# Kernel tuning notes

Hardware: AMD Instinct MI355X
Metric: run time of the kernel (lower is better)

The kernel has to match this reference:

```python
import jax, jax.numpy as jnp
import numpy as np

B, S, H = 4, 2048, 1024
NH = 16
HD = H // NH  # 64


def setup_inputs() -> dict:
    key = jax.random.key(0)
    ks = jax.random.split(key, 9)
    s = 1.0 / np.sqrt(H)
    inp = {
        "x": jax.random.normal(ks[0], (B, S, H), dtype=jnp.float32),
        "wq": jax.random.normal(ks[1], (H, H), dtype=jnp.float32) * s,
        "bq": jnp.zeros((H,), dtype=jnp.float32),
        "wk": jax.random.normal(ks[2], (H, H), dtype=jnp.float32) * s,
        "bk": jnp.zeros((H,), dtype=jnp.float32),
        "wv": jax.random.normal(ks[3], (H, H), dtype=jnp.float32) * s,
        "bv": jnp.zeros((H,), dtype=jnp.float32),
        "wo": jax.random.normal(ks[4], (H, H), dtype=jnp.float32) * s,
        "bo": jnp.zeros((H,), dtype=jnp.float32),
    }
    return inp


def _split_heads(t):
    # [B,S,H] -> [B,NH,S,HD]
    return t.reshape(B, S, NH, HD).transpose(0, 2, 1, 3)


def reference(x, wq, bq, wk, bk, wv, bv, wo, bo):
    # Linear layers (torch Linear: x @ W^T + b; weights here stored as [in,out])
    q = _split_heads(x @ wq + bq)
    k = _split_heads(x @ wk + bk)
    v = _split_heads(x @ wv + bv)
    scale = 1.0 / jnp.sqrt(jnp.asarray(HD, dtype=x.dtype))
    scores = jnp.einsum("bhqd,bhkd->bhqk", q, k) * scale  # [B,NH,S,S]
    attn = jax.nn.softmax(scores, axis=-1)
    ctx = jnp.einsum("bhqk,bhkd->bhqd", attn, v)  # [B,NH,S,HD]
    ctx = ctx.transpose(0, 2, 1, 3).reshape(B, S, H)
    return ctx @ wo + bo
```

## Files before the change

kernel.cpp:

```cpp
#include <hip/hip_runtime.h>
#include <hip/hip_bf16.h>
#include <math.h>

typedef __bf16 bf16;
typedef __attribute__((ext_vector_type(4))) __bf16 bf16x4;
typedef __attribute__((ext_vector_type(8))) __bf16 bf16x8;
typedef __attribute__((ext_vector_type(4))) float f32x4;

#define B_  4
#define S_  2048
#define H_  1024
#define NH_ 16
#define HD_ 64
#define M_  (B_ * S_)

#define LP  72
#define LPV 136
#define KV_ 128

__device__ __forceinline__ f32x4 mfma16(bf16x8 a, bf16x8 b, f32x4 c) {
    return __builtin_amdgcn_mfma_f32_16x16x32_bf16(a, b, c, 0, 0, 0);
}

__device__ __forceinline__ void glds16(const bf16* g, bf16* l) {
    __builtin_amdgcn_global_load_lds(
        (const __attribute__((address_space(1))) void*)g,
        (__attribute__((address_space(3))) void*)l, 16, 0, 0);
}

__global__ __launch_bounds__(256) void cvt_bf16(const float* __restrict__ in,
                                                bf16* __restrict__ out) {
    const size_t i = ((size_t)blockIdx.x * 256 + threadIdx.x) * 8;
    float4 f0 = *(const float4*)&in[i];
    float4 f1 = *(const float4*)&in[i + 4];
    bf16x8 v;
    v[0] = (bf16)f0.x; v[1] = (bf16)f0.y; v[2] = (bf16)f0.z; v[3] = (bf16)f0.w;
    v[4] = (bf16)f1.x; v[5] = (bf16)f1.y; v[6] = (bf16)f1.z; v[7] = (bf16)f1.w;
    *(bf16x8*)&out[i] = v;
}

__global__ __launch_bounds__(256) void transpose_w4(const float* __restrict__ s0,
                                                    const float* __restrict__ s1,
                                                    const float* __restrict__ s2,
                                                    const float* __restrict__ s3,
                                                    bf16* __restrict__ d0,
                                                    bf16* __restrict__ d1,
                                                    bf16* __restrict__ d2,
                                                    bf16* __restrict__ d3) {
    __shared__ bf16 tile[64][65];
    const int z = blockIdx.z;
    const float* in = (z == 0) ? s0 : (z == 1) ? s1 : (z == 2) ? s2 : s3;
    bf16* out = (z == 0) ? d0 : (z == 1) ? d1 : (z == 2) ? d2 : d3;
    const int t = threadIdx.x;
    const int bx = blockIdx.x * 64, by = blockIdx.y * 64;
#pragma unroll
    for (int i = 0; i < 16; ++i) {
        int idx = i * 256 + t;
        int r = idx >> 6, c = idx & 63;
        tile[r][c] = (bf16)in[(by + r) * 1024 + bx + c];
    }
    __syncthreads();
#pragma unroll
    for (int i = 0; i < 16; ++i) {
        int idx = i * 256 + t;
        int r = idx >> 6, c = idx & 63;
        out[(bx + r) * 1024 + by + c] = tile[c][r];
    }
}

__global__ __launch_bounds__(256) void gemm_qkv(const bf16* __restrict__ A,
                                                const bf16* __restrict__ Bt,
                                                const float* __restrict__ b0,
                                                const float* __restrict__ b1,
                                                const float* __restrict__ b2,
                                                bf16* __restrict__ out0,
                                                bf16* __restrict__ out1,
                                                bf16* __restrict__ out2t,
                                                float scale0) {
    __shared__ alignas(16) bf16 As[128 * 64];
    __shared__ alignas(16) bf16 Bs[128 * 64];
    const int t = threadIdx.x;
    const int m0 = blockIdx.x * 128;
    const int n0 = blockIdx.y * 128;
    const int lane = t & 63, w = t >> 6;
    const int quad = lane >> 4, l15 = lane & 15;
    const int wm = w >> 1, wn = w & 1;
    const int srow = lane >> 3;
    const int scol = (lane & 7) * 8;

    const bf16* Ab = A + (size_t)(m0 + srow) * 1024 + scol;
    const bf16* Bb = Bt + (size_t)(n0 + srow) * 1024 + scol;

    f32x4 acc[4][4];
#pragma unroll
    for (int i = 0; i < 4; ++i)
#pragma unroll
        for (int j = 0; j < 4; ++j) acc[i][j] = (f32x4){0.f, 0.f, 0.f, 0.f};

    for (int kt = 0; kt < 16; ++kt) {
#pragma unroll
        for (int i = 0; i < 4; ++i) {
            const int c = w * 4 + i;
            glds16(Ab + (size_t)c * 8 * 1024 + kt * 64, &As[c * 512]);
            glds16(Bb + (size_t)c * 8 * 1024 + kt * 64, &Bs[c * 512]);
        }
        __syncthreads();
#pragma unroll
        for (int ks = 0; ks < 2; ++ks) {
            bf16x8 a[4], b[4];
#pragma unroll
            for (int mi = 0; mi < 4; ++mi)
                a[mi] = *(const bf16x8*)&As[(wm * 64 + mi * 16 + l15) * 64 + ks * 32 + quad * 8];
#pragma unroll
            for (int ni = 0; ni < 4; ++ni)
                b[ni] = *(const bf16x8*)&Bs[(wn * 64 + ni * 16 + l15) * 64 + ks * 32 + quad * 8];
#pragma unroll
            for (int mi = 0; mi < 4; ++mi)
#pragma unroll
                for (int ni = 0; ni < 4; ++ni)
                    acc[mi][ni] = mfma16(a[mi], b[ni], acc[mi][ni]);
        }
        __syncthreads();
    }

    const int seg = n0 >> 10;
    const float* bias = (seg == 0) ? b0 : (seg == 1) ? b1 : b2;
#pragma unroll
    for (int ni = 0; ni < 4; ++ni) {
        const int coln = (n0 & 1023) + wn * 64 + ni * 16 + l15;
        const float bcol = bias[coln];
#pragma unroll
        for (int mi = 0; mi < 4; ++mi) {
            const int row0 = m0 + wm * 64 + mi * 16 + quad * 4;
            if (seg == 2) {
                bf16x4 v;
#pragma unroll
                for (int r = 0; r < 4; ++r) v[r] = (bf16)(acc[mi][ni][r] + bcol);
                *(bf16x4*)&out2t[(size_t)coln * M_ + row0] = v;
            } else if (seg == 1) {
#pragma unroll
                for (int r = 0; r < 4; ++r)
                    out1[(size_t)(row0 + r) * 1024 + coln] = (bf16)(acc[mi][ni][r] + bcol);
            } else {
#pragma unroll
                for (int r = 0; r < 4; ++r)
                    out0[(size_t)(row0 + r) * 1024 + coln] =
                        (bf16)((acc[mi][ni][r] + bcol) * scale0);
            }
        }
    }
}

__global__ __launch_bounds__(256) void gemm_o(const bf16* __restrict__ A,
                                              const bf16* __restrict__ Bt,
                                              const float* __restrict__ b0,
                                              float* __restrict__ out0) {
    __shared__ alignas(16) bf16 As[128 * 64];
    __shared__ alignas(16) bf16 Bs[128 * 64];
    const int t = threadIdx.x;
    const int m0 = blockIdx.x * 128;
    const int n0 = blockIdx.y * 128;
    const int lane = t & 63, w = t >> 6;
    const int quad = lane >> 4, l15 = lane & 15;
    const int wm = w >> 1, wn = w & 1;
    const int srow = lane >> 3;
    const int scol = (lane & 7) * 8;

    const bf16* Ab = A + (size_t)(m0 + srow) * 1024 + scol;
    const bf16* Bb = Bt + (size_t)(n0 + srow) * 1024 + scol;

    f32x4 acc[4][4];
#pragma unroll
    for (int i = 0; i < 4; ++i)
#pragma unroll
        for (int j = 0; j < 4; ++j) acc[i][j] = (f32x4){0.f, 0.f, 0.f, 0.f};

    for (int kt = 0; kt < 16; ++kt) {
#pragma unroll
        for (int i = 0; i < 4; ++i) {
            const int c = w * 4 + i;
            glds16(Ab + (size_t)c * 8 * 1024 + kt * 64, &As[c * 512]);
            glds16(Bb + (size_t)c * 8 * 1024 + kt * 64, &Bs[c * 512]);
        }
        __syncthreads();
#pragma unroll
        for (int ks = 0; ks < 2; ++ks) {
            bf16x8 a[4], b[4];
#pragma unroll
            for (int mi = 0; mi < 4; ++mi)
                a[mi] = *(const bf16x8*)&As[(wm * 64 + mi * 16 + l15) * 64 + ks * 32 + quad * 8];
#pragma unroll
            for (int ni = 0; ni < 4; ++ni)
                b[ni] = *(const bf16x8*)&Bs[(wn * 64 + ni * 16 + l15) * 64 + ks * 32 + quad * 8];
#pragma unroll
            for (int mi = 0; mi < 4; ++mi)
#pragma unroll
                for (int ni = 0; ni < 4; ++ni)
                    acc[mi][ni] = mfma16(a[mi], b[ni], acc[mi][ni]);
        }
        __syncthreads();
    }

#pragma unroll
    for (int ni = 0; ni < 4; ++ni) {
        const int coln = n0 + wn * 64 + ni * 16 + l15;
        const float bcol = b0[coln];
#pragma unroll
        for (int mi = 0; mi < 4; ++mi) {
            const int row0 = m0 + wm * 64 + mi * 16 + quad * 4;
#pragma unroll
            for (int r = 0; r < 4; ++r)
                out0[(size_t)(row0 + r) * 1024 + coln] = acc[mi][ni][r] + bcol;
        }
    }
}

__global__ __launch_bounds__(256, 4) void attn(const bf16* Q,
                                               const bf16* __restrict__ K,
                                               const bf16* __restrict__ Vt,
                                               bf16* O) {
    __shared__ alignas(16) bf16 smem[128 * LP + 64 * LPV];
    bf16* Ks = smem;
    bf16* Vs = smem + 128 * LP;

    const int t = threadIdx.x;
    const int lane = t & 63, w = t >> 6;
    const int quad = lane >> 4, l15 = lane & 15;
    const int bh = blockIdx.x;
    const int q0 = blockIdx.y * 128;
    const int b = bh >> 4, h = bh & 15;
    const bf16* qp  = Q + (size_t)b * S_ * H_ + h * HD_;
    const bf16* kp  = K + (size_t)b * S_ * H_ + h * HD_;
    const bf16* vtp = Vt + (size_t)(h * HD_) * M_ + b * S_;

    const int rk = t >> 3;
    const int kc = (t & 7) * 8;
    const int skb = ((rk >> 2) & 1) * 16 + ((rk >> 3) & 3) * 4 + (rk & 3);
    const int vd0 = rk, vd1 = rk + 32;

    bf16x8 kpre[4], vpre[4];
#pragma unroll
    for (int j = 0; j < 4; ++j)
        kpre[j] = *(const bf16x8*)&kp[(size_t)(rk + 32 * j) * H_ + kc];
    vpre[0] = *(const bf16x8*)&vtp[(size_t)vd0 * M_ + kc];
    vpre[1] = *(const bf16x8*)&vtp[(size_t)vd0 * M_ + 64 + kc];
    vpre[2] = *(const bf16x8*)&vtp[(size_t)vd1 * M_ + kc];
    vpre[3] = *(const bf16x8*)&vtp[(size_t)vd1 * M_ + 64 + kc];

#pragma unroll
    for (int i = 0; i < 4; ++i) {
        int c = i * 256 + t;
        int row = c >> 3, qkc = (c & 7) * 8;
        *(bf16x8*)&smem[row * LP + qkc] =
            *(const bf16x8*)&qp[(size_t)(q0 + row) * H_ + qkc];
    }
    __syncthreads();
    bf16x8 aq[2][2];
#pragma unroll
    for (int mi = 0; mi < 2; ++mi)
#pragma unroll
        for (int ks = 0; ks < 2; ++ks)
            aq[mi][ks] = *(const bf16x8*)
                &smem[(w * 32 + mi * 16 + l15) * LP + ks * 32 + quad * 8];

    bf16x8 ones;
#pragma unroll
    for (int j = 0; j < 8; ++j) ones[j] = (bf16)1.0f;

    f32x4 o[2][4];
    f32x4 lsum[2];
#pragma unroll
    for (int mi = 0; mi < 2; ++mi) {
        lsum[mi] = (f32x4){0.f, 0.f, 0.f, 0.f};
#pragma unroll
        for (int i = 0; i < 4; ++i) o[mi][i] = (f32x4){0.f, 0.f, 0.f, 0.f};
    }

    for (int kt = 0; kt < S_ / KV_; ++kt) {
        __syncthreads();
#pragma unroll
        for (int j = 0; j < 4; ++j)
            *(bf16x8*)&Ks[(skb + 32 * j) * LP + kc] = kpre[j];
        *(bf16x8*)&Vs[vd0 * LPV + kc]      = vpre[0];
        *(bf16x8*)&Vs[vd0 * LPV + 64 + kc] = vpre[1];
        *(bf16x8*)&Vs[vd1 * LPV + kc]      = vpre[2];
        *(bf16x8*)&Vs[vd1 * LPV + 64 + kc] = vpre[3];
        __syncthreads();

        if (kt + 1 < S_ / KV_) {
            const int key1 = (kt + 1) * KV_;
#pragma unroll
            for (int j = 0; j < 4; ++j)
                kpre[j] = *(const bf16x8*)&kp[(size_t)(key1 + rk + 32 * j) * H_ + kc];
            vpre[0] = *(const bf16x8*)&vtp[(size_t)vd0 * M_ + key1 + kc];
            vpre[1] = *(const bf16x8*)&vtp[(size_t)vd0 * M_ + key1 + 64 + kc];
            vpre[2] = *(const bf16x8*)&vtp[(size_t)vd1 * M_ + key1 + kc];
            vpre[3] = *(const bf16x8*)&vtp[(size_t)vd1 * M_ + key1 + 64 + kc];
        }

#pragma unroll
        for (int ks = 0; ks < 4; ++ks) {
            bf16x8 k00 = *(const bf16x8*)&Ks[((2 * ks) * 16 + l15) * LP + quad * 8];
            bf16x8 k01 = *(const bf16x8*)&Ks[((2 * ks) * 16 + l15) * LP + 32 + quad * 8];
            bf16x8 k10 = *(const bf16x8*)&Ks[((2 * ks + 1) * 16 + l15) * LP + quad * 8];
            bf16x8 k11 = *(const bf16x8*)&Ks[((2 * ks + 1) * 16 + l15) * LP + 32 + quad * 8];
            f32x4 sA[2], sB[2];
#pragma unroll
            for (int mi = 0; mi < 2; ++mi) {
                sA[mi] = mfma16(k00, aq[mi][0], (f32x4){0.f, 0.f, 0.f, 0.f});
                sA[mi] = mfma16(k01, aq[mi][1], sA[mi]);
                sB[mi] = mfma16(k10, aq[mi][0], (f32x4){0.f, 0.f, 0.f, 0.f});
                sB[mi] = mfma16(k11, aq[mi][1], sB[mi]);
            }
            bf16x8 ap[2];
#pragma unroll
            for (int mi = 0; mi < 2; ++mi) {
                bf16x8 v;
#pragma unroll
                for (int j = 0; j < 4; ++j) v[j] = (bf16)__expf(sA[mi][j]);
#pragma unroll
                for (int j = 0; j < 4; ++j) v[4 + j] = (bf16)__expf(sB[mi][j]);
                ap[mi] = v;
            }
#pragma unroll
            for (int mi = 0; mi < 2; ++mi)
                lsum[mi] = mfma16(ap[mi], ones, lsum[mi]);
#pragma unroll
            for (int dt = 0; dt < 4; ++dt) {
                bf16x8 bv = *(const bf16x8*)&Vs[(dt * 16 + l15) * LPV + ks * 32 + quad * 8];
#pragma unroll
                for (int mi = 0; mi < 2; ++mi)
                    o[mi][dt] = mfma16(ap[mi], bv, o[mi][dt]);
            }
        }
    }

#pragma unroll
    for (int mi = 0; mi < 2; ++mi)
#pragma unroll
        for (int r = 0; r < 4; ++r) {
            float inv = 1.f / lsum[mi][r];
            int row = q0 + w * 32 + mi * 16 + quad * 4 + r;
            size_t base = (size_t)b * S_ * H_ + (size_t)row * H_ + h * HD_;
#pragma unroll
            for (int dt = 0; dt < 4; ++dt)
                O[base + dt * 16 + l15] = (bf16)(o[mi][dt][r] * inv);
        }
}

extern "C" void kernel_launch(void* const* d_in, const int* in_sizes, int n_in,
                              void* d_out, int out_size, void* d_ws, size_t ws_size,
                              hipStream_t stream) {
    const float* x  = (const float*)d_in[0];
    const float* wq = (const float*)d_in[1];
    const float* bq = (const float*)d_in[2];
    const float* wk = (const float*)d_in[3];
    const float* bk = (const float*)d_in[4];
    const float* wv = (const float*)d_in[5];
    const float* bv = (const float*)d_in[6];
    const float* wo = (const float*)d_in[7];
    const float* bo = (const float*)d_in[8];

    bf16* ws = (bf16*)d_ws;
    const size_t WSZ = 1024 * 1024;
    const size_t TSZ = (size_t)M_ * H_;
    bf16* wt  = ws;
    bf16* qb  = wt + WSZ;
    bf16* kb  = qb + TSZ;
    bf16* vbt = kb + TSZ;
    bf16* ctx = qb;

    bf16* xb    = (bf16*)d_out;
    bf16* wqkvt = xb + TSZ;

    cvt_bf16<<<dim3(M_ * H_ / (256 * 8)), 256, 0, stream>>>(x, xb);

    transpose_w4<<<dim3(16, 16, 4), 256, 0, stream>>>(
        wq, wk, wv, wo, wqkvt, wqkvt + WSZ, wqkvt + 2 * WSZ, wt);

    dim3 qkvgrid(M_ / 128, 3072 / 128);
    gemm_qkv<<<qkvgrid, 256, 0, stream>>>(xb, wqkvt, bq, bk, bv,
                                          qb, kb, vbt, 0.125f);

    dim3 agrid(B_ * NH_, S_ / 128);
    attn<<<agrid, 256, 0, stream>>>(qb, kb, vbt, ctx);

    dim3 ogrid(M_ / 128, 1024 / 128);
    gemm_o<<<ogrid, 256, 0, stream>>>(ctx, wt, bo, (float*)d_out);
}
```

Baseline: 280.9 us.

## Double-buffer 64-key attention tiles, use exp2 with folded log2e, add setprio

The attention kernel drops from 128-key single-buffered tiles with two barriers per iteration to 64-key tiles in a double-buffered LDS ring with one barrier per iteration. The Q scale now folds in log2(e) so softmax can use exp2 instead of expf. s_setprio raises wave priority around the MFMA phases. This aims to cut barrier stalls and exponent cost, but doubles the number of loop iterations.

Result: slower. 309.5 us (+10.2%).

```diff
diff --git a/kernel.cpp b/kernel.cpp
--- a/kernel.cpp
+++ b/kernel.cpp
@@ -14,9 +14,7 @@
 #define HD_ 64
 #define M_  (B_ * S_)
 
-#define LP  72
-#define LPV 136
-#define KV_ 128
+#define LP 72
 
 __device__ __forceinline__ f32x4 mfma16(bf16x8 a, bf16x8 b, f32x4 c) {
     return __builtin_amdgcn_mfma_f32_16x16x32_bf16(a, b, c, 0, 0, 0);
@@ -219,9 +217,7 @@
                                                const bf16* __restrict__ K,
                                                const bf16* __restrict__ Vt,
                                                bf16* O) {
-    __shared__ alignas(16) bf16 smem[128 * LP + 64 * LPV];
-    bf16* Ks = smem;
-    bf16* Vs = smem + 128 * LP;
+    __shared__ alignas(16) bf16 smem[2 * 128 * LP];
 
     const int t = threadIdx.x;
     const int lane = t & 63, w = t >> 6;
@@ -233,19 +229,16 @@
     const bf16* kp  = K + (size_t)b * S_ * H_ + h * HD_;
     const bf16* vtp = Vt + (size_t)(h * HD_) * M_ + b * S_;
 
-    const int rk = t >> 3;
+    const int r0 = t >> 3, r1 = 32 + (t >> 3);
     const int kc = (t & 7) * 8;
-    const int skb = ((rk >> 2) & 1) * 16 + ((rk >> 3) & 3) * 4 + (rk & 3);
-    const int vd0 = rk, vd1 = rk + 32;
-
-    bf16x8 kpre[4], vpre[4];
-#pragma unroll
-    for (int j = 0; j < 4; ++j)
-        kpre[j] = *(const bf16x8*)&kp[(size_t)(rk + 32 * j) * H_ + kc];
-    vpre[0] = *(const bf16x8*)&vtp[(size_t)vd0 * M_ + kc];
-    vpre[1] = *(const bf16x8*)&vtp[(size_t)vd0 * M_ + 64 + kc];
-    vpre[2] = *(const bf16x8*)&vtp[(size_t)vd1 * M_ + kc];
-    vpre[3] = *(const bf16x8*)&vtp[(size_t)vd1 * M_ + 64 + kc];
+    const int s0 = ((((r0 >> 4) & 2) | ((r0 >> 2) & 1)) << 4) + (((r0 >> 3) & 3) << 2) + (r0 & 3);
+    const int s1 = ((((r1 >> 4) & 2) | ((r1 >> 2) & 1)) << 4) + (((r1 >> 3) & 3) << 2) + (r1 & 3);
+
+    bf16x8 kn[2], vn[2];
+    kn[0] = *(const bf16x8*)&kp[(size_t)r0 * H_ + kc];
+    kn[1] = *(const bf16x8*)&kp[(size_t)r1 * H_ + kc];
+    vn[0] = *(const bf16x8*)&vtp[(size_t)r0 * M_ + kc];
+    vn[1] = *(const bf16x8*)&vtp[(size_t)r1 * M_ + kc];
 
 #pragma unroll
     for (int i = 0; i < 4; ++i) {
@@ -262,6 +255,17 @@
         for (int ks = 0; ks < 2; ++ks)
             aq[mi][ks] = *(const bf16x8*)
                 &smem[(w * 32 + mi * 16 + l15) * LP + ks * 32 + quad * 8];
+    __syncthreads();
+
+    {
+        bf16* Ks0 = smem;
+        bf16* Vs0 = smem + 64 * LP;
+        *(bf16x8*)&Ks0[s0 * LP + kc] = kn[0];
+        *(bf16x8*)&Ks0[s1 * LP + kc] = kn[1];
+        *(bf16x8*)&Vs0[r0 * LP + kc] = vn[0];
+        *(bf16x8*)&Vs0[r1 * LP + kc] = vn[1];
+    }
+    __syncthreads();
 
     bf16x8 ones;
 #pragma unroll
@@ -276,62 +280,70 @@
         for (int i = 0; i < 4; ++i) o[mi][i] = (f32x4){0.f, 0.f, 0.f, 0.f};
     }
 
-    for (int kt = 0; kt < S_ / KV_; ++kt) {
-        __syncthreads();
-#pragma unroll
-        for (int j = 0; j < 4; ++j)
-            *(bf16x8*)&Ks[(skb + 32 * j) * LP + kc] = kpre[j];
-        *(bf16x8*)&Vs[vd0 * LPV + kc]      = vpre[0];
-        *(bf16x8*)&Vs[vd0 * LPV + 64 + kc] = vpre[1];
-        *(bf16x8*)&Vs[vd1 * LPV + kc]      = vpre[2];
-        *(bf16x8*)&Vs[vd1 * LPV + 64 + kc] = vpre[3];
-        __syncthreads();
-
-        if (kt + 1 < S_ / KV_) {
-            const int key1 = (kt + 1) * KV_;
-#pragma unroll
-            for (int j = 0; j < 4; ++j)
-                kpre[j] = *(const bf16x8*)&kp[(size_t)(key1 + rk + 32 * j) * H_ + kc];
-            vpre[0] = *(const bf16x8*)&vtp[(size_t)vd0 * M_ + key1 + kc];
-            vpre[1] = *(const bf16x8*)&vtp[(size_t)vd0 * M_ + key1 + 64 + kc];
-            vpre[2] = *(const bf16x8*)&vtp[(size_t)vd1 * M_ + key1 + kc];
-            vpre[3] = *(const bf16x8*)&vtp[(size_t)vd1 * M_ + key1 + 64 + kc];
-        }
-
-#pragma unroll
-        for (int ks = 0; ks < 4; ++ks) {
-            bf16x8 k00 = *(const bf16x8*)&Ks[((2 * ks) * 16 + l15) * LP + quad * 8];
-            bf16x8 k01 = *(const bf16x8*)&Ks[((2 * ks) * 16 + l15) * LP + 32 + quad * 8];
-            bf16x8 k10 = *(const bf16x8*)&Ks[((2 * ks + 1) * 16 + l15) * LP + quad * 8];
-            bf16x8 k11 = *(const bf16x8*)&Ks[((2 * ks + 1) * 16 + l15) * LP + 32 + quad * 8];
-            f32x4 sA[2], sB[2];
+    for (int kt = 0; kt < S_ / 64; ++kt) {
+        bf16* Ksc = smem + (kt & 1) * 128 * LP;
+        bf16* Vsc = Ksc + 64 * LP;
+        const bool more = (kt + 1 < S_ / 64);
+
+        if (more) {
+            const int key1 = (kt + 1) * 64;
+            kn[0] = *(const bf16x8*)&kp[(size_t)(key1 + r0) * H_ + kc];
+            kn[1] = *(const bf16x8*)&kp[(size_t)(key1 + r1) * H_ + kc];
+            vn[0] = *(const bf16x8*)&vtp[(size_t)r0 * M_ + key1 + kc];
+            vn[1] = *(const bf16x8*)&vtp[(size_t)r1 * M_ + key1 + kc];
+        }
+
+        f32x4 scT[2][4];
+        __builtin_amdgcn_s_setprio(1);
+#pragma unroll
+        for (int kb = 0; kb < 4; ++kb) {
+            bf16x8 k0 = *(const bf16x8*)&Ksc[(kb * 16 + l15) * LP + quad * 8];
+            bf16x8 k1 = *(const bf16x8*)&Ksc[(kb * 16 + l15) * LP + 32 + quad * 8];
 #pragma unroll
             for (int mi = 0; mi < 2; ++mi) {
-                sA[mi] = mfma16(k00, aq[mi][0], (f32x4){0.f, 0.f, 0.f, 0.f});
-                sA[mi] = mfma16(k01, aq[mi][1], sA[mi]);
-                sB[mi] = mfma16(k10, aq[mi][0], (f32x4){0.f, 0.f, 0.f, 0.f});
-                sB[mi] = mfma16(k11, aq[mi][1], sB[mi]);
+                scT[mi][kb] = mfma16(k0, aq[mi][0], (f32x4){0.f, 0.f, 0.f, 0.f});
+                scT[mi][kb] = mfma16(k1, aq[mi][1], scT[mi][kb]);
             }
-            bf16x8 ap[2];
-#pragma unroll
-            for (int mi = 0; mi < 2; ++mi) {
+        }
+        __builtin_amdgcn_s_setprio(0);
+
+        bf16x8 ap[2][2];
+#pragma unroll
+        for (int mi = 0; mi < 2; ++mi)
+#pragma unroll
+            for (int ks = 0; ks < 2; ++ks) {
                 bf16x8 v;
 #pragma unroll
-                for (int j = 0; j < 4; ++j) v[j] = (bf16)__expf(sA[mi][j]);
-#pragma unroll
-                for (int j = 0; j < 4; ++j) v[4 + j] = (bf16)__expf(sB[mi][j]);
-                ap[mi] = v;
+                for (int j = 0; j < 4; ++j) v[j] = (bf16)__builtin_exp2f(scT[mi][2 * ks][j]);
+#pragma unroll
+                for (int j = 0; j < 4; ++j) v[4 + j] = (bf16)__builtin_exp2f(scT[mi][2 * ks + 1][j]);
+                ap[mi][ks] = v;
             }
+
+        __builtin_amdgcn_s_setprio(1);
+#pragma unroll
+        for (int ks = 0; ks < 2; ++ks) {
 #pragma unroll
             for (int mi = 0; mi < 2; ++mi)
-                lsum[mi] = mfma16(ap[mi], ones, lsum[mi]);
+                lsum[mi] = mfma16(ap[mi][ks], ones, lsum[mi]);
 #pragma unroll
             for (int dt = 0; dt < 4; ++dt) {
-                bf16x8 bv = *(const bf16x8*)&Vs[(dt * 16 + l15) * LPV + ks * 32 + quad * 8];
+                bf16x8 bv = *(const bf16x8*)&Vsc[(dt * 16 + l15) * LP + ks * 32 + quad * 8];
 #pragma unroll
                 for (int mi = 0; mi < 2; ++mi)
-                    o[mi][dt] = mfma16(ap[mi], bv, o[mi][dt]);
+                    o[mi][dt] = mfma16(ap[mi][ks], bv, o[mi][dt]);
             }
+        }
+        __builtin_amdgcn_s_setprio(0);
+
+        if (more) {
+            bf16* Ksn = smem + ((kt + 1) & 1) * 128 * LP;
+            bf16* Vsn = Ksn + 64 * LP;
+            *(bf16x8*)&Ksn[s0 * LP + kc] = kn[0];
+            *(bf16x8*)&Ksn[s1 * LP + kc] = kn[1];
+            *(bf16x8*)&Vsn[r0 * LP + kc] = vn[0];
+            *(bf16x8*)&Vsn[r1 * LP + kc] = vn[1];
+            __syncthreads();
         }
     }
 
@@ -380,7 +392,7 @@
 
     dim3 qkvgrid(M_ / 128, 3072 / 128);
     gemm_qkv<<<qkvgrid, 256, 0, stream>>>(xb, wqkvt, bq, bk, bv,
-                                          qb, kb, vbt, 0.125f);
+                                          qb, kb, vbt, 0.18033688011112042f);
 
     dim3 agrid(B_ * NH_, S_ / 128);
     attn<<<agrid, 256, 0, stream>>>(qb, kb, vbt, ctx);
```
